# Kernel tuning notes

Hardware: AMD Instinct MI355X
Metric: run time of the kernel (lower is better)

The kernel has to match this reference:

```python
import jax, jax.numpy as jnp
import numpy as np

NUM_HEADS = 16
MASKED_BIAS = -10000.0


def setup_inputs() -> dict:
    key = jax.random.key(0)
    k1, k2, k3 = jax.random.split(key, 3)
    B, S, D = 2, 2048, 1024
    return {
        "hidden_states": jax.random.normal(k1, (B, S, D), dtype=jnp.float32),
        "c_attn_w": jax.random.normal(k2, (D, 3 * D), dtype=jnp.float32) * 0.02,
        "c_attn_b": jnp.zeros((3 * D,), dtype=jnp.float32),
        "c_proj_w": jax.random.normal(k3, (D, D), dtype=jnp.float32) * 0.02,
        "c_proj_b": jnp.zeros((D,), dtype=jnp.float32),
    }


def reference(hidden_states, c_attn_w, c_attn_b, c_proj_w, c_proj_b):
    B, S, D = hidden_states.shape
    H = NUM_HEADS
    hd = D // H

    qkv = hidden_states @ c_attn_w + c_attn_b  # [B, S, 3D]
    q, k, v = jnp.split(qkv, 3, axis=-1)

    def split_heads(t):
        return t.reshape(B, S, H, hd).transpose(0, 2, 1, 3)  # [B, H, S, hd]

    q, k, v = split_heads(q), split_heads(k), split_heads(v)

    attn_weights = jnp.einsum("bhqd,bhkd->bhqk", q, k)
    attn_weights = attn_weights / jnp.sqrt(jnp.float32(hd))
    # multiplicative causal mask, matching eager GPT2: w*mask + (-1e4)*(1-mask)
    causal = jnp.tril(jnp.ones((S, S), dtype=attn_weights.dtype))  # [S, S]
    attn_weights = attn_weights * causal + MASKED_BIAS * (1.0 - causal)
    attn_weights = jax.nn.softmax(attn_weights, axis=-1)

    attn_output = jnp.einsum("bhqk,bhkd->bhqd", attn_weights, v)
    attn_output = attn_output.transpose(0, 2, 1, 3).reshape(B, S, D)
    attn_output = attn_output @ c_proj_w + c_proj_b
    return attn_output, attn_weights
```

## Files before the change

kernel.cpp:

```cpp
#include <hip/hip_runtime.h>


typedef __bf16 bf16_t;
typedef bf16_t bf16x8 __attribute__((ext_vector_type(8)));
typedef float f32x4 __attribute__((ext_vector_type(4)));
typedef unsigned short ushort8 __attribute__((ext_vector_type(8)));
typedef unsigned short ushort4v __attribute__((ext_vector_type(4)));

#define SEQ 2048
#define DMODEL 1024
#define MTOT 4096

#define AS1 __attribute__((address_space(1)))
#define AS3 __attribute__((address_space(3)))

__device__ __forceinline__ unsigned short f2bf(float f) {
  return __builtin_bit_cast(unsigned short, (bf16_t)f);
}
__device__ __forceinline__ float bf2f(unsigned short u) {
  return __builtin_bit_cast(float, (unsigned)u << 16);
}
__device__ __forceinline__ bf16x8 ldb8(const unsigned short* p) {
  return __builtin_bit_cast(bf16x8, *(const ushort8*)p);
}
__device__ __forceinline__ f32x4 mfma16(bf16x8 a, bf16x8 b, f32x4 c) {
  return __builtin_amdgcn_mfma_f32_16x16x32_bf16(a, b, c, 0, 0, 0);
}
__device__ __forceinline__ void gload16(const unsigned short* g, unsigned short* l) {
  __builtin_amdgcn_global_load_lds((AS1 const void*)g, (AS3 void*)l, 16, 0, 0);
}

__global__ __launch_bounds__(256) void cast_kernel(const float* __restrict__ in,
                                                   unsigned short* __restrict__ out) {
  int i = blockIdx.x * 256 + threadIdx.x;
  float4 v = ((const float4*)in)[i];
  ushort4v o;
  o[0] = f2bf(v.x); o[1] = f2bf(v.y); o[2] = f2bf(v.z); o[3] = f2bf(v.w);
  ((ushort4v*)out)[i] = o;
}

__global__ __launch_bounds__(256) void transpose_cast_kernel(const float* __restrict__ in,
                                                             unsigned short* __restrict__ out,
                                                             int R, int C) {
  __shared__ float tile[32][33];
  int c0 = blockIdx.x * 32, r0 = blockIdx.y * 32;
  int tx = threadIdx.x & 31, ty = threadIdx.x >> 5;
#pragma unroll
  for (int i = 0; i < 4; ++i)
    tile[ty + i * 8][tx] = in[(size_t)(r0 + ty + i * 8) * C + c0 + tx];
  __syncthreads();
#pragma unroll
  for (int i = 0; i < 4; ++i)
    out[(size_t)(c0 + ty + i * 8) * R + r0 + tx] = f2bf(tile[tx][ty + i * 8]);
}

template <int EPI>
__global__ __launch_bounds__(256) void gemm128(
    const unsigned short* __restrict__ A, const unsigned short* __restrict__ BT,
    const float* __restrict__ bias, float* __restrict__ outF,
    unsigned short* __restrict__ qws, unsigned short* __restrict__ kws,
    unsigned short* __restrict__ vws, int M, int N, int K) {
  __shared__ unsigned short Alds[128 * 32];
  __shared__ unsigned short Blds[128 * 32];
  int m0 = blockIdx.x * 128, n0 = blockIdx.y * 128;
  int t = threadIdx.x;
  int l = t & 63, j = l & 15, g = l >> 4;
  int w = t >> 6, wr = w >> 1, wc = w & 1;

  f32x4 acc[4][4];
#pragma unroll
  for (int mi = 0; mi < 4; ++mi)
#pragma unroll
    for (int st = 0; st < 4; ++st)
#pragma unroll
      for (int r = 0; r < 4; ++r) acc[mi][st][r] = 0.f;

  int srow = t >> 2;
  int scol = (t & 3) * 8;
  const unsigned short* aB0 = A + (size_t)(m0 + srow) * K + scol;
  const unsigned short* aB1 = aB0 + (size_t)64 * K;
  const unsigned short* bB0 = BT + (size_t)(n0 + srow) * K + scol;
  const unsigned short* bB1 = bB0 + (size_t)64 * K;
  unsigned short* aL0 = &Alds[srow * 32 + scol];
  unsigned short* aL1 = aL0 + 64 * 32;
  unsigned short* bL0 = &Blds[srow * 32 + scol];
  unsigned short* bL1 = bL0 + 64 * 32;

  for (int k0 = 0; k0 < K; k0 += 32) {
    __syncthreads();
    gload16(aB0 + k0, aL0);
    gload16(aB1 + k0, aL1);
    gload16(bB0 + k0, bL0);
    gload16(bB1 + k0, bL1);
    __syncthreads();
    bf16x8 af[4], bfr[4];
#pragma unroll
    for (int mi = 0; mi < 4; ++mi) af[mi] = ldb8(&Alds[(wr * 64 + mi * 16 + j) * 32 + g * 8]);
#pragma unroll
    for (int st = 0; st < 4; ++st) bfr[st] = ldb8(&Blds[(wc * 64 + st * 16 + j) * 32 + g * 8]);
#pragma unroll
    for (int mi = 0; mi < 4; ++mi)
#pragma unroll
      for (int st = 0; st < 4; ++st) acc[mi][st] = mfma16(af[mi], bfr[st], acc[mi][st]);
  }

#pragma unroll
  for (int st = 0; st < 4; ++st) {
    int n = n0 + wc * 64 + st * 16 + j;
    float bv = bias[n];
#pragma unroll
    for (int mi = 0; mi < 4; ++mi)
#pragma unroll
      for (int r = 0; r < 4; ++r) {
        int m = m0 + wr * 64 + mi * 16 + g * 4 + r;
        float val = acc[mi][st][r] + bv;
        if (EPI == 1) {
          outF[(size_t)m * N + n] = val;
        } else {
          int region = n >> 10;
          int h = (n & 1023) >> 6;
          int d = n & 63;
          int bb = m >> 11, s = m & 2047;
          int bh = bb * 16 + h;
          if (region == 0) qws[(((size_t)bh) * SEQ + s) * 64 + d] = f2bf(val * 0.125f);
          else if (region == 1) kws[(((size_t)bh) * SEQ + s) * 64 + d] = f2bf(val);
          else vws[(((size_t)bh) * 64 + d) * SEQ + s] = f2bf(val);
        }
      }
  }
}

__global__ __launch_bounds__(256) void attn_kernel(
    const unsigned short* __restrict__ qg, const unsigned short* __restrict__ kg,
    const unsigned short* __restrict__ vg, float* __restrict__ outw,
    unsigned short* __restrict__ ointer) {
  __shared__ unsigned short Klds[64][72];
  __shared__ unsigned short Vlds[64][72];
  __shared__ unsigned short Plds[4][16][72];

  int qt = (gridDim.x - 1) - blockIdx.x;
  int bh = blockIdx.y;
  int b = bh >> 4, h = bh & 15;
  int t = threadIdx.x;
  int w = t >> 6, l = t & 63, j = l & 15, g = l >> 4;

  const unsigned short* qb = qg + (size_t)bh * SEQ * 64;
  const unsigned short* kb = kg + (size_t)bh * SEQ * 64;
  const unsigned short* vb = vg + (size_t)bh * SEQ * 64;
  float* outrow = outw + (size_t)bh * SEQ * SEQ;

  int qr_a = qt * 64 + w * 16 + j;
  bf16x8 qa0 = ldb8(&qb[(size_t)qr_a * 64 + g * 8]);
  bf16x8 qa1 = ldb8(&qb[(size_t)qr_a * 64 + 32 + g * 8]);

  int qrow0 = qt * 64 + w * 16 + g * 4;

  float lpart[4] = {0.f, 0.f, 0.f, 0.f};

  int skey = t >> 2;
  int sc = (t & 3) * 8;

  for (int kt = 0; kt <= qt; ++kt) {
    __syncthreads();
    {
      const unsigned short* src = &kb[(size_t)(kt * 64 + skey) * 64];
      *(ushort8*)&Klds[skey][sc] = *(const ushort8*)&src[sc];
      *(ushort8*)&Klds[skey][sc + 32] = *(const ushort8*)&src[sc + 32];
    }
    __syncthreads();
    f32x4 sacc[4];
#pragma unroll
    for (int st = 0; st < 4; ++st)
#pragma unroll
      for (int r = 0; r < 4; ++r) sacc[st][r] = 0.f;
#pragma unroll
    for (int st = 0; st < 4; ++st) {
      bf16x8 kf0 = ldb8(&Klds[st * 16 + j][g * 8]);
      bf16x8 kf1 = ldb8(&Klds[st * 16 + j][32 + g * 8]);
      sacc[st] = mfma16(qa0, kf0, sacc[st]);
      sacc[st] = mfma16(qa1, kf1, sacc[st]);
    }
    bool diag = (kt == qt);
#pragma unroll
    for (int r = 0; r < 4; ++r) {
      int qrow = qrow0 + r;
#pragma unroll
      for (int st = 0; st < 4; ++st) {
        float p = __expf(sacc[st][r]);
        if (diag) {
          int kc = kt * 64 + st * 16 + j;
          p = (kc > qrow) ? 0.f : p;
        }
        lpart[r] += p;
      }
    }
  }

  float linv[4];
#pragma unroll
  for (int r = 0; r < 4; ++r) {
    float sum = lpart[r];
#pragma unroll
    for (int o = 1; o < 16; o <<= 1) sum += __shfl_xor(sum, o);
    linv[r] = 1.f / sum;
  }

  f32x4 oacc[4];
#pragma unroll
  for (int st = 0; st < 4; ++st)
#pragma unroll
    for (int r = 0; r < 4; ++r) oacc[st][r] = 0.f;

  int prow = l >> 2;
  int pch = l & 3;

  for (int kt = 0; kt < SEQ / 64; ++kt) {
    if (kt <= qt) {
      __syncthreads();
      {
        const unsigned short* src = &kb[(size_t)(kt * 64 + skey) * 64];
        *(ushort8*)&Klds[skey][sc] = *(const ushort8*)&src[sc];
        *(ushort8*)&Klds[skey][sc + 32] = *(const ushort8*)&src[sc + 32];
        const unsigned short* vsrc = &vb[(size_t)skey * SEQ + kt * 64];
        *(ushort8*)&Vlds[skey][sc] = *(const ushort8*)&vsrc[sc];
        *(ushort8*)&Vlds[skey][sc + 32] = *(const ushort8*)&vsrc[sc + 32];
      }
      __syncthreads();
      f32x4 sacc[4];
#pragma unroll
      for (int st = 0; st < 4; ++st)
#pragma unroll
        for (int r = 0; r < 4; ++r) sacc[st][r] = 0.f;
#pragma unroll
      for (int st = 0; st < 4; ++st) {
        bf16x8 kf0 = ldb8(&Klds[st * 16 + j][g * 8]);
        bf16x8 kf1 = ldb8(&Klds[st * 16 + j][32 + g * 8]);
        sacc[st] = mfma16(qa0, kf0, sacc[st]);
        sacc[st] = mfma16(qa1, kf1, sacc[st]);
      }
      bool diag = (kt == qt);
#pragma unroll
      for (int st = 0; st < 4; ++st) {
#pragma unroll
        for (int r = 0; r < 4; ++r) {
          int qrow = qrow0 + r;
          int kc = kt * 64 + st * 16 + j;
          float p = __expf(sacc[st][r]) * linv[r];
          if (diag) p = (kc > qrow) ? 0.f : p;
          Plds[w][g * 4 + r][st * 16 + j] = f2bf(p);
        }
      }
#pragma unroll
      for (int it = 0; it < 2; ++it) {
        int ch = pch + it * 4;
        ushort8 pv = *(const ushort8*)&Plds[w][prow][ch * 8];
        float4 f0, f1;
        f0.x = bf2f(pv[0]); f0.y = bf2f(pv[1]); f0.z = bf2f(pv[2]); f0.w = bf2f(pv[3]);
        f1.x = bf2f(pv[4]); f1.y = bf2f(pv[5]); f1.z = bf2f(pv[6]); f1.w = bf2f(pv[7]);
        float* dst = &outrow[(size_t)(qt * 64 + w * 16 + prow) * SEQ + kt * 64 + ch * 8];
        ((float4*)dst)[0] = f0;
        ((float4*)dst)[1] = f1;
      }
      bf16x8 pa0 = ldb8(&Plds[w][j][g * 8]);
      bf16x8 pa1 = ldb8(&Plds[w][j][32 + g * 8]);
#pragma unroll
      for (int st = 0; st < 4; ++st) {
        bf16x8 vf0 = ldb8(&Vlds[st * 16 + j][g * 8]);
        bf16x8 vf1 = ldb8(&Vlds[st * 16 + j][32 + g * 8]);
        oacc[st] = mfma16(pa0, vf0, oacc[st]);
        oacc[st] = mfma16(pa1, vf1, oacc[st]);
      }
    } else {
      int row = qt * 64 + w * 16 + (l >> 2);
      int c0 = kt * 64 + (l & 3) * 16;
      float4 z = make_float4(0.f, 0.f, 0.f, 0.f);
      float4* zp = (float4*)&outrow[(size_t)row * SEQ + c0];
      zp[0] = z; zp[1] = z; zp[2] = z; zp[3] = z;
    }
  }

#pragma unroll
  for (int st = 0; st < 4; ++st)
#pragma unroll
    for (int r = 0; r < 4; ++r) {
      int qrow = qrow0 + r;
      int d = st * 16 + j;
      ointer[((size_t)b * SEQ + qrow) * DMODEL + h * 64 + d] = f2bf(oacc[st][r]);
    }
}

extern "C" void kernel_launch(void* const* d_in, const int* in_sizes, int n_in,
                              void* d_out, int out_size, void* d_ws, size_t ws_size,
                              hipStream_t stream) {
  const float* hidden = (const float*)d_in[0];
  const float* w_attn = (const float*)d_in[1];
  const float* b_attn = (const float*)d_in[2];
  const float* w_proj = (const float*)d_in[3];
  const float* b_proj = (const float*)d_in[4];

  float* out_attn = (float*)d_out;
  float* out_w = out_attn + (size_t)MTOT * DMODEL;

  char* ws = (char*)d_ws;
  unsigned short* hbf = (unsigned short*)(ws);
  unsigned short* w1T = (unsigned short*)(ws + 8388608);
  unsigned short* w2T = (unsigned short*)(ws + 14680064);
  unsigned short* qws = (unsigned short*)(ws + 16777216);
  unsigned short* kws = (unsigned short*)(ws + 25165824);
  unsigned short* vws = (unsigned short*)(ws + 33554432);

  cast_kernel<<<4096, 256, 0, stream>>>(hidden, hbf);
  transpose_cast_kernel<<<dim3(96, 32), 256, 0, stream>>>(w_attn, w1T, 1024, 3072);
  transpose_cast_kernel<<<dim3(32, 32), 256, 0, stream>>>(w_proj, w2T, 1024, 1024);
  gemm128<0><<<dim3(32, 24), 256, 0, stream>>>(hbf, w1T, b_attn, nullptr, qws, kws, vws,
                                               MTOT, 3 * DMODEL, DMODEL);
  attn_kernel<<<dim3(32, 32), 256, 0, stream>>>(qws, kws, vws, out_w, hbf);
  gemm128<1><<<dim3(32, 8), 256, 0, stream>>>(hbf, w2T, b_proj, out_attn, nullptr, nullptr,
                                              nullptr, MTOT, DMODEL, DMODEL);
}
```

Measured before the change: 273.2 us.

## Double-buffer K tiles with async direct-to-LDS loads and XOR-swizzled layout

Rewrites attention K/V staging to use gload16 (presumably global-to-LDS direct loads defined in the hidden helpers) into an XOR-swizzled unpadded layout, with K double-buffered so the next tile's load overlaps the current tile's MFMAs. The masked-region zero-fill is moved out of the main loop to after the output write. Launch bounds now request 4 blocks per CU. It aims to hide global load latency and cut LDS bank conflicts and sync overhead. The cost is more LDS use and tighter register limits.

```diff
diff --git a/kernel.cpp b/kernel.cpp
--- a/kernel.cpp
+++ b/kernel.cpp
@@ -130,13 +130,13 @@
   }
 }
 
-__global__ __launch_bounds__(256) void attn_kernel(
+__global__ __launch_bounds__(256, 4) void attn_kernel(
     const unsigned short* __restrict__ qg, const unsigned short* __restrict__ kg,
     const unsigned short* __restrict__ vg, float* __restrict__ outw,
     unsigned short* __restrict__ ointer) {
-  __shared__ unsigned short Klds[64][72];
-  __shared__ unsigned short Vlds[64][72];
-  __shared__ unsigned short Plds[4][16][72];
+  __shared__ unsigned short Kb[2][64 * 64];
+  __shared__ unsigned short Vb[64 * 64];
+  __shared__ unsigned short Plds[4][16 * 72];
 
   int qt = (gridDim.x - 1) - blockIdx.x;
   int bh = blockIdx.y;
@@ -155,19 +155,36 @@
 
   int qrow0 = qt * 64 + w * 16 + g * 4;
 
+  int srow = t >> 3;
+  int swz8 = ((t & 7) ^ (srow & 7)) * 8;
+  const unsigned short* ksrc0 = kb + srow * 64 + swz8;
+  const unsigned short* ksrc1 = ksrc0 + 32 * 64;
+  const unsigned short* vsrc0 = vb + (size_t)srow * SEQ + swz8;
+  const unsigned short* vsrc1 = vsrc0 + (size_t)32 * SEQ;
+  unsigned short* kd0a = &Kb[0][t * 8];
+  unsigned short* kd1a = kd0a + 2048;
+  unsigned short* kd0b = &Kb[1][t * 8];
+  unsigned short* kd1b = kd0b + 2048;
+  unsigned short* vd0 = &Vb[t * 8];
+  unsigned short* vd1 = vd0 + 2048;
+
+  int rb0 = j * 64 + ((g ^ (j & 7)) * 8);
+  int rb1 = j * 64 + (((4 + g) ^ (j & 7)) * 8);
+
   float lpart[4] = {0.f, 0.f, 0.f, 0.f};
 
-  int skey = t >> 2;
-  int sc = (t & 3) * 8;
-
+  gload16(ksrc0, kd0a);
+  gload16(ksrc1, kd1a);
+  __syncthreads();
   for (int kt = 0; kt <= qt; ++kt) {
-    __syncthreads();
-    {
-      const unsigned short* src = &kb[(size_t)(kt * 64 + skey) * 64];
-      *(ushort8*)&Klds[skey][sc] = *(const ushort8*)&src[sc];
-      *(ushort8*)&Klds[skey][sc + 32] = *(const ushort8*)&src[sc + 32];
-    }
-    __syncthreads();
+    const unsigned short* KbC = Kb[kt & 1];
+    if (kt < qt) {
+      const unsigned short* s0 = ksrc0 + (kt + 1) * 4096;
+      unsigned short* dA = (kt & 1) ? kd0a : kd0b;
+      unsigned short* dB = (kt & 1) ? kd1a : kd1b;
+      gload16(s0, dA);
+      gload16(s0 + 32 * 64, dB);
+    }
     f32x4 sacc[4];
 #pragma unroll
     for (int st = 0; st < 4; ++st)
@@ -175,8 +192,8 @@
       for (int r = 0; r < 4; ++r) sacc[st][r] = 0.f;
 #pragma unroll
     for (int st = 0; st < 4; ++st) {
-      bf16x8 kf0 = ldb8(&Klds[st * 16 + j][g * 8]);
-      bf16x8 kf1 = ldb8(&Klds[st * 16 + j][32 + g * 8]);
+      bf16x8 kf0 = ldb8(KbC + st * 1024 + rb0);
+      bf16x8 kf1 = ldb8(KbC + st * 1024 + rb1);
       sacc[st] = mfma16(qa0, kf0, sacc[st]);
       sacc[st] = mfma16(qa1, kf1, sacc[st]);
     }
@@ -194,6 +211,7 @@
         lpart[r] += p;
       }
     }
+    __syncthreads();
   }
 
   float linv[4];
@@ -214,69 +232,66 @@
   int prow = l >> 2;
   int pch = l & 3;
 
-  for (int kt = 0; kt < SEQ / 64; ++kt) {
-    if (kt <= qt) {
-      __syncthreads();
-      {
-        const unsigned short* src = &kb[(size_t)(kt * 64 + skey) * 64];
-        *(ushort8*)&Klds[skey][sc] = *(const ushort8*)&src[sc];
-        *(ushort8*)&Klds[skey][sc + 32] = *(const ushort8*)&src[sc + 32];
-        const unsigned short* vsrc = &vb[(size_t)skey * SEQ + kt * 64];
-        *(ushort8*)&Vlds[skey][sc] = *(const ushort8*)&vsrc[sc];
-        *(ushort8*)&Vlds[skey][sc + 32] = *(const ushort8*)&vsrc[sc + 32];
+  gload16(ksrc0, kd0a);
+  gload16(ksrc1, kd1a);
+  __syncthreads();
+  for (int kt = 0; kt <= qt; ++kt) {
+    const unsigned short* KbC = Kb[kt & 1];
+    gload16(vsrc0 + kt * 64, vd0);
+    gload16(vsrc1 + kt * 64, vd1);
+    if (kt < qt) {
+      const unsigned short* s0 = ksrc0 + (kt + 1) * 4096;
+      unsigned short* dA = (kt & 1) ? kd0a : kd0b;
+      unsigned short* dB = (kt & 1) ? kd1a : kd1b;
+      gload16(s0, dA);
+      gload16(s0 + 32 * 64, dB);
+    }
+    f32x4 sacc[4];
+#pragma unroll
+    for (int st = 0; st < 4; ++st)
+#pragma unroll
+      for (int r = 0; r < 4; ++r) sacc[st][r] = 0.f;
+#pragma unroll
+    for (int st = 0; st < 4; ++st) {
+      bf16x8 kf0 = ldb8(KbC + st * 1024 + rb0);
+      bf16x8 kf1 = ldb8(KbC + st * 1024 + rb1);
+      sacc[st] = mfma16(qa0, kf0, sacc[st]);
+      sacc[st] = mfma16(qa1, kf1, sacc[st]);
+    }
+    bool diag = (kt == qt);
+#pragma unroll
+    for (int st = 0; st < 4; ++st) {
+#pragma unroll
+      for (int r = 0; r < 4; ++r) {
+        int qrow = qrow0 + r;
+        int kc = kt * 64 + st * 16 + j;
+        float p = __expf(sacc[st][r]) * linv[r];
+        if (diag) p = (kc > qrow) ? 0.f : p;
+        Plds[w][(g * 4 + r) * 72 + st * 16 + j] = f2bf(p);
       }
-      __syncthreads();
-      f32x4 sacc[4];
-#pragma unroll
-      for (int st = 0; st < 4; ++st)
-#pragma unroll
-        for (int r = 0; r < 4; ++r) sacc[st][r] = 0.f;
-#pragma unroll
-      for (int st = 0; st < 4; ++st) {
-        bf16x8 kf0 = ldb8(&Klds[st * 16 + j][g * 8]);
-        bf16x8 kf1 = ldb8(&Klds[st * 16 + j][32 + g * 8]);
-        sacc[st] = mfma16(qa0, kf0, sacc[st]);
-        sacc[st] = mfma16(qa1, kf1, sacc[st]);
-      }
-      bool diag = (kt == qt);
-#pragma unroll
-      for (int st = 0; st < 4; ++st) {
-#pragma unroll
-        for (int r = 0; r < 4; ++r) {
-          int qrow = qrow0 + r;
-          int kc = kt * 64 + st * 16 + j;
-          float p = __expf(sacc[st][r]) * linv[r];
-          if (diag) p = (kc > qrow) ? 0.f : p;
-          Plds[w][g * 4 + r][st * 16 + j] = f2bf(p);
-        }
-      }
-#pragma unroll
-      for (int it = 0; it < 2; ++it) {
-        int ch = pch + it * 4;
-        ushort8 pv = *(const ushort8*)&Plds[w][prow][ch * 8];
-        float4 f0, f1;
-        f0.x = bf2f(pv[0]); f0.y = bf2f(pv[1]); f0.z = bf2f(pv[2]); f0.w = bf2f(pv[3]);
-        f1.x = bf2f(pv[4]); f1.y = bf2f(pv[5]); f1.z = bf2f(pv[6]); f1.w = bf2f(pv[7]);
-        float* dst = &outrow[(size_t)(qt * 64 + w * 16 + prow) * SEQ + kt * 64 + ch * 8];
-        ((float4*)dst)[0] = f0;
-        ((float4*)dst)[1] = f1;
-      }
-      bf16x8 pa0 = ldb8(&Plds[w][j][g * 8]);
-      bf16x8 pa1 = ldb8(&Plds[w][j][32 + g * 8]);
-#pragma unroll
-      for (int st = 0; st < 4; ++st) {
-        bf16x8 vf0 = ldb8(&Vlds[st * 16 + j][g * 8]);
-        bf16x8 vf1 = ldb8(&Vlds[st * 16 + j][32 + g * 8]);
-        oacc[st] = mfma16(pa0, vf0, oacc[st]);
-        oacc[st] = mfma16(pa1, vf1, oacc[st]);
-      }
-    } else {
-      int row = qt * 64 + w * 16 + (l >> 2);
-      int c0 = kt * 64 + (l & 3) * 16;
-      float4 z = make_float4(0.f, 0.f, 0.f, 0.f);
-      float4* zp = (float4*)&outrow[(size_t)row * SEQ + c0];
-      zp[0] = z; zp[1] = z; zp[2] = z; zp[3] = z;
-    }
+    }
+#pragma unroll
+    for (int it = 0; it < 2; ++it) {
+      int ch = pch + it * 4;
+      ushort8 pv = *(const ushort8*)&Plds[w][prow * 72 + ch * 8];
+      float4 f0, f1;
+      f0.x = bf2f(pv[0]); f0.y = bf2f(pv[1]); f0.z = bf2f(pv[2]); f0.w = bf2f(pv[3]);
+      f1.x = bf2f(pv[4]); f1.y = bf2f(pv[5]); f1.z = bf2f(pv[6]); f1.w = bf2f(pv[7]);
+      float* dst = &outrow[(size_t)(qt * 64 + w * 16 + prow) * SEQ + kt * 64 + ch * 8];
+      ((float4*)dst)[0] = f0;
+      ((float4*)dst)[1] = f1;
+    }
+    __syncthreads();
+    bf16x8 pa0 = ldb8(&Plds[w][j * 72 + g * 8]);
+    bf16x8 pa1 = ldb8(&Plds[w][j * 72 + 32 + g * 8]);
+#pragma unroll
+    for (int st = 0; st < 4; ++st) {
+      bf16x8 vf0 = ldb8(Vb + st * 1024 + rb0);
+      bf16x8 vf1 = ldb8(Vb + st * 1024 + rb1);
+      oacc[st] = mfma16(pa0, vf0, oacc[st]);
+      oacc[st] = mfma16(pa1, vf1, oacc[st]);
+    }
+    __syncthreads();
   }
 
 #pragma unroll
@@ -287,6 +302,14 @@
       int d = st * 16 + j;
       ointer[((size_t)b * SEQ + qrow) * DMODEL + h * 64 + d] = f2bf(oacc[st][r]);
     }
+
+  for (int kt = qt + 1; kt < SEQ / 64; ++kt) {
+    int row = qt * 64 + w * 16 + (l >> 2);
+    int c0 = kt * 64 + (l & 3) * 16;
+    float4 z = make_float4(0.f, 0.f, 0.f, 0.f);
+    float4* zp = (float4*)&outrow[(size_t)row * SEQ + c0];
+    zp[0] = z; zp[1] = z; zp[2] = z; zp[3] = z;
+  }
 }
 
 extern "C" void kernel_launch(void* const* d_in, const int* in_sizes, int n_in,
```

Result: slower. 623.3 us (+128.1%).

## Pair short and long causal query tiles per block and prefetch K/V into registers

Applied to the files above, without the earlier changes.

Each attention block now handles two query tiles, qtA and 31-qtA, so every block does the same amount of causal work, and the grid shrinks from 32 to 16 tiles per head. The two tiles share each K and V tile staged in LDS, which halves K/V global loads. The next K/V tile is prefetched into registers while the current one is computed. Zero-filling of the masked upper triangle moves after the compute loop. The cost is fewer blocks in flight (512), higher register pressure from two sets of accumulators, and serialised per-tile work inside a block.

```diff
diff --git a/kernel.cpp b/kernel.cpp
--- a/kernel.cpp
+++ b/kernel.cpp
@@ -136,9 +136,10 @@
     unsigned short* __restrict__ ointer) {
   __shared__ unsigned short Klds[64][72];
   __shared__ unsigned short Vlds[64][72];
-  __shared__ unsigned short Plds[4][16][72];
-
-  int qt = (gridDim.x - 1) - blockIdx.x;
+  __shared__ unsigned short Plds[4][16 * 72];
+
+  int qtA = blockIdx.x;
+  int qtB = 31 - qtA;
   int bh = blockIdx.y;
   int b = bh >> 4, h = bh & 15;
   int t = threadIdx.x;
@@ -149,83 +150,122 @@
   const unsigned short* vb = vg + (size_t)bh * SEQ * 64;
   float* outrow = outw + (size_t)bh * SEQ * SEQ;
 
-  int qr_a = qt * 64 + w * 16 + j;
-  bf16x8 qa0 = ldb8(&qb[(size_t)qr_a * 64 + g * 8]);
-  bf16x8 qa1 = ldb8(&qb[(size_t)qr_a * 64 + 32 + g * 8]);
-
-  int qrow0 = qt * 64 + w * 16 + g * 4;
-
-  float lpart[4] = {0.f, 0.f, 0.f, 0.f};
+  int qrA_a = qtA * 64 + w * 16 + j;
+  int qrB_a = qtB * 64 + w * 16 + j;
+  bf16x8 qaA0 = ldb8(&qb[(size_t)qrA_a * 64 + g * 8]);
+  bf16x8 qaA1 = ldb8(&qb[(size_t)qrA_a * 64 + 32 + g * 8]);
+  bf16x8 qaB0 = ldb8(&qb[(size_t)qrB_a * 64 + g * 8]);
+  bf16x8 qaB1 = ldb8(&qb[(size_t)qrB_a * 64 + 32 + g * 8]);
+
+  int qrow0A = qtA * 64 + w * 16 + g * 4;
+  int qrow0B = qtB * 64 + w * 16 + g * 4;
 
   int skey = t >> 2;
   int sc = (t & 3) * 8;
 
-  for (int kt = 0; kt <= qt; ++kt) {
-    __syncthreads();
-    {
-      const unsigned short* src = &kb[(size_t)(kt * 64 + skey) * 64];
-      *(ushort8*)&Klds[skey][sc] = *(const ushort8*)&src[sc];
-      *(ushort8*)&Klds[skey][sc + 32] = *(const ushort8*)&src[sc + 32];
-    }
-    __syncthreads();
-    f32x4 sacc[4];
+  float lpartA[4] = {0.f, 0.f, 0.f, 0.f};
+  float lpartB[4] = {0.f, 0.f, 0.f, 0.f};
+
+  ushort8 kr0 = *(const ushort8*)&kb[(size_t)skey * 64 + sc];
+  ushort8 kr1 = *(const ushort8*)&kb[(size_t)skey * 64 + sc + 32];
+  for (int kt = 0; kt <= qtB; ++kt) {
+    __syncthreads();
+    *(ushort8*)&Klds[skey][sc] = kr0;
+    *(ushort8*)&Klds[skey][sc + 32] = kr1;
+    __syncthreads();
+    if (kt < qtB) {
+      const unsigned short* nsrc = &kb[(size_t)((kt + 1) * 64 + skey) * 64];
+      kr0 = *(const ushort8*)&nsrc[sc];
+      kr1 = *(const ushort8*)&nsrc[sc + 32];
+    }
+    bool doA = (kt <= qtA);
+    f32x4 sA[4], sB[4];
 #pragma unroll
     for (int st = 0; st < 4; ++st)
 #pragma unroll
-      for (int r = 0; r < 4; ++r) sacc[st][r] = 0.f;
+      for (int r = 0; r < 4; ++r) { sA[st][r] = 0.f; sB[st][r] = 0.f; }
 #pragma unroll
     for (int st = 0; st < 4; ++st) {
       bf16x8 kf0 = ldb8(&Klds[st * 16 + j][g * 8]);
       bf16x8 kf1 = ldb8(&Klds[st * 16 + j][32 + g * 8]);
-      sacc[st] = mfma16(qa0, kf0, sacc[st]);
-      sacc[st] = mfma16(qa1, kf1, sacc[st]);
-    }
-    bool diag = (kt == qt);
+      sB[st] = mfma16(qaB0, kf0, sB[st]);
+      sB[st] = mfma16(qaB1, kf1, sB[st]);
+      if (doA) {
+        sA[st] = mfma16(qaA0, kf0, sA[st]);
+        sA[st] = mfma16(qaA1, kf1, sA[st]);
+      }
+    }
+    bool diagB = (kt == qtB);
 #pragma unroll
     for (int r = 0; r < 4; ++r) {
-      int qrow = qrow0 + r;
 #pragma unroll
       for (int st = 0; st < 4; ++st) {
-        float p = __expf(sacc[st][r]);
-        if (diag) {
+        float p = __expf(sB[st][r]);
+        if (diagB) {
           int kc = kt * 64 + st * 16 + j;
-          p = (kc > qrow) ? 0.f : p;
+          p = (kc > qrow0B + r) ? 0.f : p;
         }
-        lpart[r] += p;
-      }
-    }
-  }
-
-  float linv[4];
+        lpartB[r] += p;
+      }
+    }
+    if (doA) {
+      bool diagA = (kt == qtA);
+#pragma unroll
+      for (int r = 0; r < 4; ++r) {
+#pragma unroll
+        for (int st = 0; st < 4; ++st) {
+          float p = __expf(sA[st][r]);
+          if (diagA) {
+            int kc = kt * 64 + st * 16 + j;
+            p = (kc > qrow0A + r) ? 0.f : p;
+          }
+          lpartA[r] += p;
+        }
+      }
+    }
+  }
+
+  float linvA[4], linvB[4];
 #pragma unroll
   for (int r = 0; r < 4; ++r) {
-    float sum = lpart[r];
-#pragma unroll
-    for (int o = 1; o < 16; o <<= 1) sum += __shfl_xor(sum, o);
-    linv[r] = 1.f / sum;
-  }
-
-  f32x4 oacc[4];
+    float sa = lpartA[r], sb = lpartB[r];
+#pragma unroll
+    for (int o = 1; o < 16; o <<= 1) { sa += __shfl_xor(sa, o); sb += __shfl_xor(sb, o); }
+    linvA[r] = 1.f / sa;
+    linvB[r] = 1.f / sb;
+  }
+
+  f32x4 oaccA[4], oaccB[4];
 #pragma unroll
   for (int st = 0; st < 4; ++st)
 #pragma unroll
-    for (int r = 0; r < 4; ++r) oacc[st][r] = 0.f;
+    for (int r = 0; r < 4; ++r) { oaccA[st][r] = 0.f; oaccB[st][r] = 0.f; }
 
   int prow = l >> 2;
   int pch = l & 3;
 
-  for (int kt = 0; kt < SEQ / 64; ++kt) {
-    if (kt <= qt) {
-      __syncthreads();
-      {
-        const unsigned short* src = &kb[(size_t)(kt * 64 + skey) * 64];
-        *(ushort8*)&Klds[skey][sc] = *(const ushort8*)&src[sc];
-        *(ushort8*)&Klds[skey][sc + 32] = *(const ushort8*)&src[sc + 32];
-        const unsigned short* vsrc = &vb[(size_t)skey * SEQ + kt * 64];
-        *(ushort8*)&Vlds[skey][sc] = *(const ushort8*)&vsrc[sc];
-        *(ushort8*)&Vlds[skey][sc + 32] = *(const ushort8*)&vsrc[sc + 32];
-      }
-      __syncthreads();
+  kr0 = *(const ushort8*)&kb[(size_t)skey * 64 + sc];
+  kr1 = *(const ushort8*)&kb[(size_t)skey * 64 + sc + 32];
+  ushort8 vr0 = *(const ushort8*)&vb[(size_t)skey * SEQ + sc];
+  ushort8 vr1 = *(const ushort8*)&vb[(size_t)skey * SEQ + sc + 32];
+  for (int kt = 0; kt <= qtB; ++kt) {
+    __syncthreads();
+    *(ushort8*)&Klds[skey][sc] = kr0;
+    *(ushort8*)&Klds[skey][sc + 32] = kr1;
+    *(ushort8*)&Vlds[skey][sc] = vr0;
+    *(ushort8*)&Vlds[skey][sc + 32] = vr1;
+    __syncthreads();
+    if (kt < qtB) {
+      const unsigned short* nk = &kb[(size_t)((kt + 1) * 64 + skey) * 64];
+      const unsigned short* nv = &vb[(size_t)skey * SEQ + (kt + 1) * 64];
+      kr0 = *(const ushort8*)&nk[sc];
+      kr1 = *(const ushort8*)&nk[sc + 32];
+      vr0 = *(const ushort8*)&nv[sc];
+      vr1 = *(const ushort8*)&nv[sc + 32];
+    }
+    bool doA = (kt <= qtA);
+
+    {
       f32x4 sacc[4];
 #pragma unroll
       for (int st = 0; st < 4; ++st)
@@ -235,58 +275,110 @@
       for (int st = 0; st < 4; ++st) {
         bf16x8 kf0 = ldb8(&Klds[st * 16 + j][g * 8]);
         bf16x8 kf1 = ldb8(&Klds[st * 16 + j][32 + g * 8]);
-        sacc[st] = mfma16(qa0, kf0, sacc[st]);
-        sacc[st] = mfma16(qa1, kf1, sacc[st]);
-      }
-      bool diag = (kt == qt);
-#pragma unroll
-      for (int st = 0; st < 4; ++st) {
+        sacc[st] = mfma16(qaB0, kf0, sacc[st]);
+        sacc[st] = mfma16(qaB1, kf1, sacc[st]);
+      }
+      bool diag = (kt == qtB);
+#pragma unroll
+      for (int st = 0; st < 4; ++st)
 #pragma unroll
         for (int r = 0; r < 4; ++r) {
-          int qrow = qrow0 + r;
           int kc = kt * 64 + st * 16 + j;
-          float p = __expf(sacc[st][r]) * linv[r];
-          if (diag) p = (kc > qrow) ? 0.f : p;
-          Plds[w][g * 4 + r][st * 16 + j] = f2bf(p);
+          float p = __expf(sacc[st][r]) * linvB[r];
+          if (diag) p = (kc > qrow0B + r) ? 0.f : p;
+          Plds[w][(g * 4 + r) * 72 + st * 16 + j] = f2bf(p);
         }
-      }
 #pragma unroll
       for (int it = 0; it < 2; ++it) {
         int ch = pch + it * 4;
-        ushort8 pv = *(const ushort8*)&Plds[w][prow][ch * 8];
+        ushort8 pv = *(const ushort8*)&Plds[w][prow * 72 + ch * 8];
         float4 f0, f1;
         f0.x = bf2f(pv[0]); f0.y = bf2f(pv[1]); f0.z = bf2f(pv[2]); f0.w = bf2f(pv[3]);
         f1.x = bf2f(pv[4]); f1.y = bf2f(pv[5]); f1.z = bf2f(pv[6]); f1.w = bf2f(pv[7]);
-        float* dst = &outrow[(size_t)(qt * 64 + w * 16 + prow) * SEQ + kt * 64 + ch * 8];
+        float* dst = &outrow[(size_t)(qtB * 64 + w * 16 + prow) * SEQ + kt * 64 + ch * 8];
         ((float4*)dst)[0] = f0;
         ((float4*)dst)[1] = f1;
       }
-      bf16x8 pa0 = ldb8(&Plds[w][j][g * 8]);
-      bf16x8 pa1 = ldb8(&Plds[w][j][32 + g * 8]);
+      bf16x8 pa0 = ldb8(&Plds[w][j * 72 + g * 8]);
+      bf16x8 pa1 = ldb8(&Plds[w][j * 72 + 32 + g * 8]);
 #pragma unroll
       for (int st = 0; st < 4; ++st) {
         bf16x8 vf0 = ldb8(&Vlds[st * 16 + j][g * 8]);
         bf16x8 vf1 = ldb8(&Vlds[st * 16 + j][32 + g * 8]);
-        oacc[st] = mfma16(pa0, vf0, oacc[st]);
-        oacc[st] = mfma16(pa1, vf1, oacc[st]);
-      }
-    } else {
-      int row = qt * 64 + w * 16 + (l >> 2);
-      int c0 = kt * 64 + (l & 3) * 16;
-      float4 z = make_float4(0.f, 0.f, 0.f, 0.f);
-      float4* zp = (float4*)&outrow[(size_t)row * SEQ + c0];
+        oaccB[st] = mfma16(pa0, vf0, oaccB[st]);
+        oaccB[st] = mfma16(pa1, vf1, oaccB[st]);
+      }
+    }
+
+    if (doA) {
+      f32x4 sacc[4];
+#pragma unroll
+      for (int st = 0; st < 4; ++st)
+#pragma unroll
+        for (int r = 0; r < 4; ++r) sacc[st][r] = 0.f;
+#pragma unroll
+      for (int st = 0; st < 4; ++st) {
+        bf16x8 kf0 = ldb8(&Klds[st * 16 + j][g * 8]);
+        bf16x8 kf1 = ldb8(&Klds[st * 16 + j][32 + g * 8]);
+        sacc[st] = mfma16(qaA0, kf0, sacc[st]);
+        sacc[st] = mfma16(qaA1, kf1, sacc[st]);
+      }
+      bool diag = (kt == qtA);
+#pragma unroll
+      for (int st = 0; st < 4; ++st)
+#pragma unroll
+        for (int r = 0; r < 4; ++r) {
+          int kc = kt * 64 + st * 16 + j;
+          float p = __expf(sacc[st][r]) * linvA[r];
+          if (diag) p = (kc > qrow0A + r) ? 0.f : p;
+          Plds[w][(g * 4 + r) * 72 + st * 16 + j] = f2bf(p);
+        }
+#pragma unroll
+      for (int it = 0; it < 2; ++it) {
+        int ch = pch + it * 4;
+        ushort8 pv = *(const ushort8*)&Plds[w][prow * 72 + ch * 8];
+        float4 f0, f1;
+        f0.x = bf2f(pv[0]); f0.y = bf2f(pv[1]); f0.z = bf2f(pv[2]); f0.w = bf2f(pv[3]);
+        f1.x = bf2f(pv[4]); f1.y = bf2f(pv[5]); f1.z = bf2f(pv[6]); f1.w = bf2f(pv[7]);
+        float* dst = &outrow[(size_t)(qtA * 64 + w * 16 + prow) * SEQ + kt * 64 + ch * 8];
+        ((float4*)dst)[0] = f0;
+        ((float4*)dst)[1] = f1;
+      }
+      bf16x8 pa0 = ldb8(&Plds[w][j * 72 + g * 8]);
+      bf16x8 pa1 = ldb8(&Plds[w][j * 72 + 32 + g * 8]);
+#pragma unroll
+      for (int st = 0; st < 4; ++st) {
+        bf16x8 vf0 = ldb8(&Vlds[st * 16 + j][g * 8]);
+        bf16x8 vf1 = ldb8(&Vlds[st * 16 + j][32 + g * 8]);
+        oaccA[st] = mfma16(pa0, vf0, oaccA[st]);
+        oaccA[st] = mfma16(pa1, vf1, oaccA[st]);
+      }
+    }
+  }
+
+#pragma unroll
+  for (int st = 0; st < 4; ++st)
+#pragma unroll
+    for (int r = 0; r < 4; ++r) {
+      int d = st * 16 + j;
+      ointer[((size_t)b * SEQ + qrow0A + r) * DMODEL + h * 64 + d] = f2bf(oaccA[st][r]);
+      ointer[((size_t)b * SEQ + qrow0B + r) * DMODEL + h * 64 + d] = f2bf(oaccB[st][r]);
+    }
+
+  {
+    int rowA = qtA * 64 + w * 16 + (l >> 2);
+    int rowB = qtB * 64 + w * 16 + (l >> 2);
+    int cc = (l & 3) * 16;
+    float4 z = make_float4(0.f, 0.f, 0.f, 0.f);
+    for (int kt = qtA + 1; kt < SEQ / 64; ++kt) {
+      float4* zp = (float4*)&outrow[(size_t)rowA * SEQ + kt * 64 + cc];
       zp[0] = z; zp[1] = z; zp[2] = z; zp[3] = z;
     }
-  }
-
-#pragma unroll
-  for (int st = 0; st < 4; ++st)
-#pragma unroll
-    for (int r = 0; r < 4; ++r) {
-      int qrow = qrow0 + r;
-      int d = st * 16 + j;
-      ointer[((size_t)b * SEQ + qrow) * DMODEL + h * 64 + d] = f2bf(oacc[st][r]);
-    }
+    for (int kt = qtB + 1; kt < SEQ / 64; ++kt) {
+      float4* zp = (float4*)&outrow[(size_t)rowB * SEQ + kt * 64 + cc];
+      zp[0] = z; zp[1] = z; zp[2] = z; zp[3] = z;
+    }
+  }
 }
 
 extern "C" void kernel_launch(void* const* d_in, const int* in_sizes, int n_in,
@@ -314,7 +406,7 @@
   transpose_cast_kernel<<<dim3(32, 32), 256, 0, stream>>>(w_proj, w2T, 1024, 1024);
   gemm128<0><<<dim3(32, 24), 256, 0, stream>>>(hbf, w1T, b_attn, nullptr, qws, kws, vws,
                                                MTOT, 3 * DMODEL, DMODEL);
-  attn_kernel<<<dim3(32, 32), 256, 0, stream>>>(qws, kws, vws, out_w, hbf);
+  attn_kernel<<<dim3(16, 32), 256, 0, stream>>>(qws, kws, vws, out_w, hbf);
   gemm128<1><<<dim3(32, 8), 256, 0, stream>>>(hbf, w2T, b_proj, out_attn, nullptr, nullptr,
                                               nullptr, MTOT, DMODEL, DMODEL);
 }
```

Measured after the change: 466.4 us. +70.7%, slower.

## Widen attention key tiles to 128 and prefetch K/V into registers

Applied to the files above, without the earlier changes.

The attention kernel now processes 128-key tiles per iteration instead of 64, halving the number of loop trips and barriers. It prefetches the next K and V tiles into registers while the current tile is being computed, overlapping global loads with MFMA and exp work. Zero-filling of the masked upper region moves to a separate loop after the main loop, and launch bounds request 3 blocks per CU. On the diagonal, the 128-wide tile computes and writes scores that are later masked to zero, which adds some wasted work, and the larger tiles raise register and LDS pressure.

```diff
diff --git a/kernel.cpp b/kernel.cpp
--- a/kernel.cpp
+++ b/kernel.cpp
@@ -130,19 +130,20 @@
   }
 }
 
-__global__ __launch_bounds__(256) void attn_kernel(
+__global__ __launch_bounds__(256, 3) void attn_kernel(
     const unsigned short* __restrict__ qg, const unsigned short* __restrict__ kg,
     const unsigned short* __restrict__ vg, float* __restrict__ outw,
     unsigned short* __restrict__ ointer) {
-  __shared__ unsigned short Klds[64][72];
-  __shared__ unsigned short Vlds[64][72];
-  __shared__ unsigned short Plds[4][16][72];
-
-  int qt = (gridDim.x - 1) - blockIdx.x;
+  __shared__ unsigned short Klds[128 * 72];
+  __shared__ unsigned short Vlds[64 * 136];
+  __shared__ unsigned short Plds[4 * 16 * 136];
+
+  int qt = 31 - blockIdx.x;
   int bh = blockIdx.y;
   int b = bh >> 4, h = bh & 15;
   int t = threadIdx.x;
   int w = t >> 6, l = t & 63, j = l & 15, g = l >> 4;
+  int nkt = (qt >> 1) + 1;
 
   const unsigned short* qb = qg + (size_t)bh * SEQ * 64;
   const unsigned short* kb = kg + (size_t)bh * SEQ * 64;
@@ -155,40 +156,49 @@
 
   int qrow0 = qt * 64 + w * 16 + g * 4;
 
+  int krow = t >> 1;
+  int kcol = (t & 1) * 32;
+  int vrow = t >> 2;
+  int vcol = (t & 3) * 32;
+  unsigned short* Pw = &Plds[w * (16 * 136)];
+
   float lpart[4] = {0.f, 0.f, 0.f, 0.f};
 
-  int skey = t >> 2;
-  int sc = (t & 3) * 8;
-
-  for (int kt = 0; kt <= qt; ++kt) {
-    __syncthreads();
-    {
-      const unsigned short* src = &kb[(size_t)(kt * 64 + skey) * 64];
-      *(ushort8*)&Klds[skey][sc] = *(const ushort8*)&src[sc];
-      *(ushort8*)&Klds[skey][sc + 32] = *(const ushort8*)&src[sc + 32];
-    }
-    __syncthreads();
-    f32x4 sacc[4];
-#pragma unroll
-    for (int st = 0; st < 4; ++st)
+  ushort8 kr[4];
+#pragma unroll
+  for (int i = 0; i < 4; ++i)
+    kr[i] = *(const ushort8*)&kb[(size_t)krow * 64 + kcol + i * 8];
+  for (int kt = 0; kt < nkt; ++kt) {
+    __syncthreads();
+#pragma unroll
+    for (int i = 0; i < 4; ++i) *(ushort8*)&Klds[krow * 72 + kcol + i * 8] = kr[i];
+    __syncthreads();
+    if (kt + 1 < nkt) {
+      const unsigned short* nk = &kb[(size_t)((kt + 1) * 128 + krow) * 64 + kcol];
+#pragma unroll
+      for (int i = 0; i < 4; ++i) kr[i] = *(const ushort8*)&nk[i * 8];
+    }
+    f32x4 sacc[8];
+#pragma unroll
+    for (int st = 0; st < 8; ++st)
 #pragma unroll
       for (int r = 0; r < 4; ++r) sacc[st][r] = 0.f;
 #pragma unroll
-    for (int st = 0; st < 4; ++st) {
-      bf16x8 kf0 = ldb8(&Klds[st * 16 + j][g * 8]);
-      bf16x8 kf1 = ldb8(&Klds[st * 16 + j][32 + g * 8]);
+    for (int st = 0; st < 8; ++st) {
+      bf16x8 kf0 = ldb8(&Klds[(st * 16 + j) * 72 + g * 8]);
+      bf16x8 kf1 = ldb8(&Klds[(st * 16 + j) * 72 + 32 + g * 8]);
       sacc[st] = mfma16(qa0, kf0, sacc[st]);
       sacc[st] = mfma16(qa1, kf1, sacc[st]);
     }
-    bool diag = (kt == qt);
+    bool diag = (kt == nkt - 1);
 #pragma unroll
     for (int r = 0; r < 4; ++r) {
       int qrow = qrow0 + r;
 #pragma unroll
-      for (int st = 0; st < 4; ++st) {
+      for (int st = 0; st < 8; ++st) {
         float p = __expf(sacc[st][r]);
         if (diag) {
-          int kc = kt * 64 + st * 16 + j;
+          int kc = kt * 128 + st * 16 + j;
           p = (kc > qrow) ? 0.f : p;
         }
         lpart[r] += p;
@@ -214,69 +224,72 @@
   int prow = l >> 2;
   int pch = l & 3;
 
-  for (int kt = 0; kt < SEQ / 64; ++kt) {
-    if (kt <= qt) {
-      __syncthreads();
-      {
-        const unsigned short* src = &kb[(size_t)(kt * 64 + skey) * 64];
-        *(ushort8*)&Klds[skey][sc] = *(const ushort8*)&src[sc];
-        *(ushort8*)&Klds[skey][sc + 32] = *(const ushort8*)&src[sc + 32];
-        const unsigned short* vsrc = &vb[(size_t)skey * SEQ + kt * 64];
-        *(ushort8*)&Vlds[skey][sc] = *(const ushort8*)&vsrc[sc];
-        *(ushort8*)&Vlds[skey][sc + 32] = *(const ushort8*)&vsrc[sc + 32];
-      }
-      __syncthreads();
-      f32x4 sacc[4];
-#pragma unroll
-      for (int st = 0; st < 4; ++st)
-#pragma unroll
-        for (int r = 0; r < 4; ++r) sacc[st][r] = 0.f;
-#pragma unroll
-      for (int st = 0; st < 4; ++st) {
-        bf16x8 kf0 = ldb8(&Klds[st * 16 + j][g * 8]);
-        bf16x8 kf1 = ldb8(&Klds[st * 16 + j][32 + g * 8]);
-        sacc[st] = mfma16(qa0, kf0, sacc[st]);
-        sacc[st] = mfma16(qa1, kf1, sacc[st]);
-      }
-      bool diag = (kt == qt);
-#pragma unroll
-      for (int st = 0; st < 4; ++st) {
-#pragma unroll
-        for (int r = 0; r < 4; ++r) {
-          int qrow = qrow0 + r;
-          int kc = kt * 64 + st * 16 + j;
-          float p = __expf(sacc[st][r]) * linv[r];
-          if (diag) p = (kc > qrow) ? 0.f : p;
-          Plds[w][g * 4 + r][st * 16 + j] = f2bf(p);
-        }
-      }
-#pragma unroll
-      for (int it = 0; it < 2; ++it) {
-        int ch = pch + it * 4;
-        ushort8 pv = *(const ushort8*)&Plds[w][prow][ch * 8];
-        float4 f0, f1;
-        f0.x = bf2f(pv[0]); f0.y = bf2f(pv[1]); f0.z = bf2f(pv[2]); f0.w = bf2f(pv[3]);
-        f1.x = bf2f(pv[4]); f1.y = bf2f(pv[5]); f1.z = bf2f(pv[6]); f1.w = bf2f(pv[7]);
-        float* dst = &outrow[(size_t)(qt * 64 + w * 16 + prow) * SEQ + kt * 64 + ch * 8];
-        ((float4*)dst)[0] = f0;
-        ((float4*)dst)[1] = f1;
-      }
-      bf16x8 pa0 = ldb8(&Plds[w][j][g * 8]);
-      bf16x8 pa1 = ldb8(&Plds[w][j][32 + g * 8]);
-#pragma unroll
-      for (int st = 0; st < 4; ++st) {
-        bf16x8 vf0 = ldb8(&Vlds[st * 16 + j][g * 8]);
-        bf16x8 vf1 = ldb8(&Vlds[st * 16 + j][32 + g * 8]);
-        oacc[st] = mfma16(pa0, vf0, oacc[st]);
-        oacc[st] = mfma16(pa1, vf1, oacc[st]);
-      }
-    } else {
-      int row = qt * 64 + w * 16 + (l >> 2);
-      int c0 = kt * 64 + (l & 3) * 16;
-      float4 z = make_float4(0.f, 0.f, 0.f, 0.f);
-      float4* zp = (float4*)&outrow[(size_t)row * SEQ + c0];
-      zp[0] = z; zp[1] = z; zp[2] = z; zp[3] = z;
-    }
+  ushort8 vr[4];
+#pragma unroll
+  for (int i = 0; i < 4; ++i) {
+    kr[i] = *(const ushort8*)&kb[(size_t)krow * 64 + kcol + i * 8];
+    vr[i] = *(const ushort8*)&vb[(size_t)vrow * SEQ + vcol + i * 8];
+  }
+  for (int kt = 0; kt < nkt; ++kt) {
+    __syncthreads();
+#pragma unroll
+    for (int i = 0; i < 4; ++i) {
+      *(ushort8*)&Klds[krow * 72 + kcol + i * 8] = kr[i];
+      *(ushort8*)&Vlds[vrow * 136 + vcol + i * 8] = vr[i];
+    }
+    __syncthreads();
+    if (kt + 1 < nkt) {
+      const unsigned short* nk = &kb[(size_t)((kt + 1) * 128 + krow) * 64 + kcol];
+      const unsigned short* nv = &vb[(size_t)vrow * SEQ + (kt + 1) * 128 + vcol];
+#pragma unroll
+      for (int i = 0; i < 4; ++i) {
+        kr[i] = *(const ushort8*)&nk[i * 8];
+        vr[i] = *(const ushort8*)&nv[i * 8];
+      }
+    }
+    f32x4 sacc[8];
+#pragma unroll
+    for (int st = 0; st < 8; ++st)
+#pragma unroll
+      for (int r = 0; r < 4; ++r) sacc[st][r] = 0.f;
+#pragma unroll
+    for (int st = 0; st < 8; ++st) {
+      bf16x8 kf0 = ldb8(&Klds[(st * 16 + j) * 72 + g * 8]);
+      bf16x8 kf1 = ldb8(&Klds[(st * 16 + j) * 72 + 32 + g * 8]);
+      sacc[st] = mfma16(qa0, kf0, sacc[st]);
+      sacc[st] = mfma16(qa1, kf1, sacc[st]);
+    }
+    bool diag = (kt == nkt - 1);
+#pragma unroll
+    for (int st = 0; st < 8; ++st)
+#pragma unroll
+      for (int r = 0; r < 4; ++r) {
+        int kc = kt * 128 + st * 16 + j;
+        float p = __expf(sacc[st][r]) * linv[r];
+        if (diag) p = (kc > qrow0 + r) ? 0.f : p;
+        Pw[(g * 4 + r) * 136 + st * 16 + j] = f2bf(p);
+      }
+#pragma unroll
+    for (int it = 0; it < 4; ++it) {
+      int ch = pch + it * 4;
+      ushort8 pv = *(const ushort8*)&Pw[prow * 136 + ch * 8];
+      float4 f0, f1;
+      f0.x = bf2f(pv[0]); f0.y = bf2f(pv[1]); f0.z = bf2f(pv[2]); f0.w = bf2f(pv[3]);
+      f1.x = bf2f(pv[4]); f1.y = bf2f(pv[5]); f1.z = bf2f(pv[6]); f1.w = bf2f(pv[7]);
+      float* dst = &outrow[(size_t)(qt * 64 + w * 16 + prow) * SEQ + kt * 128 + ch * 8];
+      ((float4*)dst)[0] = f0;
+      ((float4*)dst)[1] = f1;
+    }
+    bf16x8 pa[4];
+#pragma unroll
+    for (int ks = 0; ks < 4; ++ks) pa[ks] = ldb8(&Pw[j * 136 + ks * 32 + g * 8]);
+#pragma unroll
+    for (int st = 0; st < 4; ++st)
+#pragma unroll
+      for (int ks = 0; ks < 4; ++ks) {
+        bf16x8 vf = ldb8(&Vlds[(st * 16 + j) * 136 + ks * 32 + g * 8]);
+        oacc[st] = mfma16(pa[ks], vf, oacc[st]);
+      }
   }
 
 #pragma unroll
@@ -287,6 +300,15 @@
       int d = st * 16 + j;
       ointer[((size_t)b * SEQ + qrow) * DMODEL + h * 64 + d] = f2bf(oacc[st][r]);
     }
+
+  {
+    int row = qt * 64 + w * 16 + (l >> 2);
+    float4 z = make_float4(0.f, 0.f, 0.f, 0.f);
+    for (int c0 = nkt * 128 + (l & 3) * 16; c0 < SEQ; c0 += 64) {
+      float4* zp = (float4*)&outrow[(size_t)row * SEQ + c0];
+      zp[0] = z; zp[1] = z; zp[2] = z; zp[3] = z;
+    }
+  }
 }
 
 extern "C" void kernel_launch(void* const* d_in, const int* in_sizes, int n_in,
```

Result: slower. 632.2 us (+131.4%).
